# Kernel tuning notes

Measured on AMD Instinct MI355X. Metric: run time of the kernel, lower is better.

Reference implementation:

```python
import jax, jax.numpy as jnp
import numpy as np

B, D, H, V, T = 64, 1024, 1024, 32000, 20
SOS = 0  # word_to_idx['<SOS>']


def setup_inputs() -> dict:
    key = jax.random.key(0)
    ks = jax.random.split(key, 6)
    s = 0.02
    return {
        "latent_vector": jax.random.normal(ks[0], (B, D), jnp.float32),
        "W_proj": jax.random.normal(ks[1], (H, D), jnp.float32) * s,
        "b_proj": jnp.zeros((H,), jnp.float32),
        "emb": jax.random.normal(ks[2], (V, H), jnp.float32) * s,
        "W_ih": jax.random.normal(ks[3], (3 * H, H), jnp.float32) * s,
        "b_ih": jnp.zeros((3 * H,), jnp.float32),
        "W_hh": jax.random.normal(ks[4], (3 * H, H), jnp.float32) * s,
        "b_hh": jnp.zeros((3 * H,), jnp.float32),
        "W_out": jax.random.normal(ks[5], (V, H), jnp.float32) * s,
        "b_out": jnp.zeros((V,), jnp.float32),
    }


def _gru_cell(x, h, W_ih, b_ih, W_hh, b_hh):
    # PyTorch GRU cell gate math
    gi = x @ W_ih.T + b_ih  # [B, 3H]
    gh = h @ W_hh.T + b_hh  # [B, 3H]
    i_r, i_z, i_n = jnp.split(gi, 3, axis=-1)
    h_r, h_z, h_n = jnp.split(gh, 3, axis=-1)
    r = jax.nn.sigmoid(i_r + h_r)
    z = jax.nn.sigmoid(i_z + h_z)
    n = jnp.tanh(i_n + r * h_n)
    return (1.0 - z) * n + z * h


def reference(latent_vector, W_proj, b_proj, emb, W_ih, b_ih, W_hh, b_hh, W_out, b_out):
    batch = latent_vector.shape[0]
    h = latent_vector @ W_proj.T + b_proj  # init_hidden: [B, H]
    tok0 = jnp.full((batch,), SOS, dtype=jnp.int32)

    def step(carry, _):
        tok, h = carry
        x = emb[tok]                                  # embedding lookup [B, H]
        h = _gru_cell(x, h, W_ih, b_ih, W_hh, b_hh)   # GRU step
        logits = h @ W_out.T + b_out                  # [B, V]
        tok = jnp.argmax(logits, axis=-1).astype(jnp.int32)  # topk(1) greedy
        return (tok, h), tok

    (_, h_final), toks = jax.lax.scan(step, (tok0, h), None, length=T)
    # torch: stack(outputs, dim=1).squeeze() -> [B, T]; hidden -> [1, B, H]
    return toks.T, h_final[None, :, :]
```

## Files before the change

### kernel.cpp

```cpp
#include <hip/hip_runtime.h>
#include <stdint.h>

#define B_ 64
#define D_ 1024
#define H_ 1024
#define V_ 32000
#define T_ 20

typedef __attribute__((ext_vector_type(8))) __bf16 bf16x8;
typedef __attribute__((ext_vector_type(4))) float f32x4;

__device__ __forceinline__ uint32_t ord_of_float(float x) {
    uint32_t u = __float_as_uint(x);
    return (u & 0x80000000u) ? ~u : (u | 0x80000000u);
}

__device__ __forceinline__ unsigned long long shfl_xor_u64(unsigned long long x, int m) {
    return (unsigned long long)__shfl_xor((long long)x, m, 64);
}

__device__ __forceinline__ void split_bf16(float f, unsigned short* hi, unsigned short* lo) {
    uint32_t u = __float_as_uint(f);
    uint32_t rh = (u + 0x7FFFu + ((u >> 16) & 1u)) >> 16;
    *hi = (unsigned short)rh;
    float fl = f - __uint_as_float(rh << 16);
    uint32_t ul = __float_as_uint(fl);
    uint32_t rl = (ul + 0x7FFFu + ((ul >> 16) & 1u)) >> 16;
    *lo = (unsigned short)rl;
}

__global__ __launch_bounds__(256) void k_init_hidden(
    const float* __restrict__ latent, const float* __restrict__ Wp,
    const float* __restrict__ bp, float* __restrict__ h0)
{
    int gw = (blockIdx.x * 256 + threadIdx.x) >> 6;
    int lane = threadIdx.x & 63;
    int j = gw >> 6;
    int b = gw & 63;
    const float4* a4 = (const float4*)(latent + b * D_);
    const float4* w4 = (const float4*)(Wp + (size_t)j * D_);
    float s = 0.f;
#pragma unroll
    for (int i = 0; i < 4; i++) {
        float4 a = a4[lane + 64 * i];
        float4 w = w4[lane + 64 * i];
        s += a.x * w.x + a.y * w.y + a.z * w.z + a.w * w.w;
    }
#pragma unroll
    for (int off = 32; off; off >>= 1) s += __shfl_down(s, off, 64);
    if (lane == 0) h0[b * H_ + j] = s + bp[j];
}

#define LSTRIDE 72

__global__ __launch_bounds__(256) void k_gates_gemm(
    const float* __restrict__ emb, const int* __restrict__ tok, int use_sos,
    const float* __restrict__ hprev, const float* __restrict__ Wih,
    const float* __restrict__ Whh, float* __restrict__ gbuf)
{
    __shared__ unsigned short Ahi[64 * LSTRIDE], Alo[64 * LSTRIDE];
    __shared__ unsigned short Bhi[64 * LSTRIDE], Blo[64 * LSTRIDE];
    int tid = threadIdx.x;
    int lane = tid & 63;
    int wv = tid >> 6;
    int blk = blockIdx.x;
    int jt = blk % 48;
    int rest = blk / 48;
    int half = rest & 1;
    int ks = rest >> 1;
    int kbase = ks * 512;

    const float* W = half ? Whh : Wih;

    int srow = tid >> 2;
    int scol = (tid & 3) * 16;
    const float* arow;
    if (half == 0) {
        int xr = use_sos ? 0 : tok[srow];
        arow = emb + (size_t)xr * H_;
    } else {
        arow = hprev + srow * H_;
    }
    const float* asrc = arow + kbase + scol;
    const float* bsrc = W + (size_t)(jt * 64 + srow) * H_ + kbase + scol;

    unsigned short* ahd = Ahi + srow * LSTRIDE + scol;
    unsigned short* ald = Alo + srow * LSTRIDE + scol;
    unsigned short* bhd = Bhi + srow * LSTRIDE + scol;
    unsigned short* bld = Blo + srow * LSTRIDE + scol;

    f32x4 acc[4];
#pragma unroll
    for (int i = 0; i < 4; i++) acc[i] = (f32x4){0.f, 0.f, 0.f, 0.f};

    int arow_f = wv * 16 + (lane & 15);
    int koff = (lane >> 4) * 8;

    for (int kc = 0; kc < 512; kc += 64) {
        float4 av[4], bv[4];
#pragma unroll
        for (int i = 0; i < 4; i++) {
            av[i] = *(const float4*)(asrc + kc + 4 * i);
            bv[i] = *(const float4*)(bsrc + kc + 4 * i);
        }
        __syncthreads();
#pragma unroll
        for (int i = 0; i < 4; i++) {
            split_bf16(av[i].x, ahd + 4 * i + 0, ald + 4 * i + 0);
            split_bf16(av[i].y, ahd + 4 * i + 1, ald + 4 * i + 1);
            split_bf16(av[i].z, ahd + 4 * i + 2, ald + 4 * i + 2);
            split_bf16(av[i].w, ahd + 4 * i + 3, ald + 4 * i + 3);
            split_bf16(bv[i].x, bhd + 4 * i + 0, bld + 4 * i + 0);
            split_bf16(bv[i].y, bhd + 4 * i + 1, bld + 4 * i + 1);
            split_bf16(bv[i].z, bhd + 4 * i + 2, bld + 4 * i + 2);
            split_bf16(bv[i].w, bhd + 4 * i + 3, bld + 4 * i + 3);
        }
        __syncthreads();
        bf16x8 ah0 = *(const bf16x8*)(Ahi + arow_f * LSTRIDE + koff);
        bf16x8 ah1 = *(const bf16x8*)(Ahi + arow_f * LSTRIDE + 32 + koff);
        bf16x8 al0 = *(const bf16x8*)(Alo + arow_f * LSTRIDE + koff);
        bf16x8 al1 = *(const bf16x8*)(Alo + arow_f * LSTRIDE + 32 + koff);
#pragma unroll
        for (int tv = 0; tv < 4; tv++) {
            int brow = tv * 16 + (lane & 15);
            bf16x8 bh0 = *(const bf16x8*)(Bhi + brow * LSTRIDE + koff);
            bf16x8 bh1 = *(const bf16x8*)(Bhi + brow * LSTRIDE + 32 + koff);
            bf16x8 bl0 = *(const bf16x8*)(Blo + brow * LSTRIDE + koff);
            bf16x8 bl1 = *(const bf16x8*)(Blo + brow * LSTRIDE + 32 + koff);
            acc[tv] = __builtin_amdgcn_mfma_f32_16x16x32_bf16(ah0, bh0, acc[tv], 0, 0, 0);
            acc[tv] = __builtin_amdgcn_mfma_f32_16x16x32_bf16(ah1, bh1, acc[tv], 0, 0, 0);
            acc[tv] = __builtin_amdgcn_mfma_f32_16x16x32_bf16(al0, bh0, acc[tv], 0, 0, 0);
            acc[tv] = __builtin_amdgcn_mfma_f32_16x16x32_bf16(al1, bh1, acc[tv], 0, 0, 0);
            acc[tv] = __builtin_amdgcn_mfma_f32_16x16x32_bf16(ah0, bl0, acc[tv], 0, 0, 0);
            acc[tv] = __builtin_amdgcn_mfma_f32_16x16x32_bf16(ah1, bl1, acc[tv], 0, 0, 0);
        }
    }

    int col = lane & 15;
    int quad = lane >> 4;
    float* og = gbuf + (size_t)((ks * 2 + half) * 64) * 3072;
#pragma unroll
    for (int tv = 0; tv < 4; tv++) {
#pragma unroll
        for (int r = 0; r < 4; r++) {
            int b = wv * 16 + quad * 4 + r;
            og[(size_t)b * 3072 + jt * 64 + tv * 16 + col] = acc[tv][r];
        }
    }
}

__global__ __launch_bounds__(256) void k_gru_elem(
    const float* __restrict__ gbuf, const float* __restrict__ bih,
    const float* __restrict__ bhh, const float* __restrict__ hprev,
    float* __restrict__ hnext)
{
    int idx = blockIdx.x * 256 + threadIdx.x;
    int b = idx >> 10;
    int j = idx & 1023;
    const float* g00 = gbuf + (size_t)b * 3072;
    const float* g01 = gbuf + (size_t)(64 + b) * 3072;
    const float* g10 = gbuf + (size_t)(128 + b) * 3072;
    const float* g11 = gbuf + (size_t)(192 + b) * 3072;
    float ir = g00[j] + g10[j] + bih[j];
    float hr = g01[j] + g11[j] + bhh[j];
    float iz = g00[H_ + j] + g10[H_ + j] + bih[H_ + j];
    float hz = g01[H_ + j] + g11[H_ + j] + bhh[H_ + j];
    float in_ = g00[2 * H_ + j] + g10[2 * H_ + j] + bih[2 * H_ + j];
    float hn = g01[2 * H_ + j] + g11[2 * H_ + j] + bhh[2 * H_ + j];
    float r = 1.f / (1.f + expf(-(ir + hr)));
    float z = 1.f / (1.f + expf(-(iz + hz)));
    float n = tanhf(in_ + r * hn);
    float hp = hprev[idx];
    hnext[idx] = (1.f - z) * n + z * hp;
}

__global__ __launch_bounds__(256) void k_logits_argmax(
    const float* __restrict__ hcur, const float* __restrict__ Wout,
    const float* __restrict__ bout, unsigned long long* __restrict__ partials,
    int nblk)
{
    __shared__ unsigned short Ahi[64 * LSTRIDE], Alo[64 * LSTRIDE];
    __shared__ unsigned short Bhi[64 * LSTRIDE], Blo[64 * LSTRIDE];
    int tid = threadIdx.x;
    int lane = tid & 63;
    int wv = tid >> 6;
    int vbase = blockIdx.x * 64;

    int srow = tid >> 2;
    int scol = (tid & 3) * 16;
    const float* asrc = hcur + srow * H_ + scol;
    const float* bsrc = Wout + (size_t)(vbase + srow) * H_ + scol;
    unsigned short* ahd = Ahi + srow * LSTRIDE + scol;
    unsigned short* ald = Alo + srow * LSTRIDE + scol;
    unsigned short* bhd = Bhi + srow * LSTRIDE + scol;
    unsigned short* bld = Blo + srow * LSTRIDE + scol;

    f32x4 acc[4];
#pragma unroll
    for (int i = 0; i < 4; i++) acc[i] = (f32x4){0.f, 0.f, 0.f, 0.f};

    int arow = wv * 16 + (lane & 15);
    int koff = (lane >> 4) * 8;

    for (int kc = 0; kc < H_; kc += 64) {
        float4 av[4], bv[4];
#pragma unroll
        for (int i = 0; i < 4; i++) {
            av[i] = *(const float4*)(asrc + kc + 4 * i);
            bv[i] = *(const float4*)(bsrc + kc + 4 * i);
        }
        __syncthreads();
#pragma unroll
        for (int i = 0; i < 4; i++) {
            split_bf16(av[i].x, ahd + 4 * i + 0, ald + 4 * i + 0);
            split_bf16(av[i].y, ahd + 4 * i + 1, ald + 4 * i + 1);
            split_bf16(av[i].z, ahd + 4 * i + 2, ald + 4 * i + 2);
            split_bf16(av[i].w, ahd + 4 * i + 3, ald + 4 * i + 3);
            split_bf16(bv[i].x, bhd + 4 * i + 0, bld + 4 * i + 0);
            split_bf16(bv[i].y, bhd + 4 * i + 1, bld + 4 * i + 1);
            split_bf16(bv[i].z, bhd + 4 * i + 2, bld + 4 * i + 2);
            split_bf16(bv[i].w, bhd + 4 * i + 3, bld + 4 * i + 3);
        }
        __syncthreads();
        bf16x8 ah0 = *(const bf16x8*)(Ahi + arow * LSTRIDE + koff);
        bf16x8 ah1 = *(const bf16x8*)(Ahi + arow * LSTRIDE + 32 + koff);
        bf16x8 al0 = *(const bf16x8*)(Alo + arow * LSTRIDE + koff);
        bf16x8 al1 = *(const bf16x8*)(Alo + arow * LSTRIDE + 32 + koff);
#pragma unroll
        for (int tv = 0; tv < 4; tv++) {
            int brow = tv * 16 + (lane & 15);
            bf16x8 bh0 = *(const bf16x8*)(Bhi + brow * LSTRIDE + koff);
            bf16x8 bh1 = *(const bf16x8*)(Bhi + brow * LSTRIDE + 32 + koff);
            bf16x8 bl0 = *(const bf16x8*)(Blo + brow * LSTRIDE + koff);
            bf16x8 bl1 = *(const bf16x8*)(Blo + brow * LSTRIDE + 32 + koff);
            acc[tv] = __builtin_amdgcn_mfma_f32_16x16x32_bf16(ah0, bh0, acc[tv], 0, 0, 0);
            acc[tv] = __builtin_amdgcn_mfma_f32_16x16x32_bf16(ah1, bh1, acc[tv], 0, 0, 0);
            acc[tv] = __builtin_amdgcn_mfma_f32_16x16x32_bf16(al0, bh0, acc[tv], 0, 0, 0);
            acc[tv] = __builtin_amdgcn_mfma_f32_16x16x32_bf16(al1, bh1, acc[tv], 0, 0, 0);
            acc[tv] = __builtin_amdgcn_mfma_f32_16x16x32_bf16(ah0, bl0, acc[tv], 0, 0, 0);
            acc[tv] = __builtin_amdgcn_mfma_f32_16x16x32_bf16(ah1, bl1, acc[tv], 0, 0, 0);
        }
    }

    int col = lane & 15;
    int quad = lane >> 4;
    unsigned long long kmax[4] = {0ull, 0ull, 0ull, 0ull};
#pragma unroll
    for (int tv = 0; tv < 4; tv++) {
        int v = vbase + tv * 16 + col;
        float bo = bout[v];
#pragma unroll
        for (int r = 0; r < 4; r++) {
            float lg = acc[tv][r] + bo;
            unsigned long long key = ((unsigned long long)ord_of_float(lg) << 32)
                                   | (unsigned long long)(0x7FFFFFFFu - (uint32_t)v);
            if (key > kmax[r]) kmax[r] = key;
        }
    }
#pragma unroll
    for (int r = 0; r < 4; r++) {
        unsigned long long k = kmax[r];
#pragma unroll
        for (int off = 1; off < 16; off <<= 1) {
            unsigned long long o = shfl_xor_u64(k, off);
            if (o > k) k = o;
        }
        kmax[r] = k;
    }
    if (col == 0) {
#pragma unroll
        for (int r = 0; r < 4; r++) {
            int b = wv * 16 + quad * 4 + r;
            partials[(size_t)b * nblk + blockIdx.x] = kmax[r];
        }
    }
}

__global__ __launch_bounds__(64) void k_token(
    const unsigned long long* __restrict__ partials, int nblk,
    int* __restrict__ tok, float* __restrict__ out_tokens, int t)
{
    int b = blockIdx.x;
    int lane = threadIdx.x;
    unsigned long long k = 0ull;
    for (int i = lane; i < nblk; i += 64) {
        unsigned long long p = partials[(size_t)b * nblk + i];
        if (p > k) k = p;
    }
#pragma unroll
    for (int off = 32; off; off >>= 1) {
        unsigned long long o = shfl_xor_u64(k, off);
        if (o > k) k = o;
    }
    if (lane == 0) {
        int v = (int)(0x7FFFFFFFu - (uint32_t)(k & 0xFFFFFFFFull));
        tok[b] = v;
        out_tokens[b * T_ + t] = (float)v;
    }
}

__global__ __launch_bounds__(256) void k_copy_h(const float* __restrict__ h,
                                               float* __restrict__ out)
{
    int i = (blockIdx.x * 256 + threadIdx.x) * 4;
    *(float4*)(out + i) = *(const float4*)(h + i);
}

extern "C" void kernel_launch(void* const* d_in, const int* in_sizes, int n_in,
                              void* d_out, int out_size, void* d_ws, size_t ws_size,
                              hipStream_t stream)
{
    const float* latent = (const float*)d_in[0];
    const float* Wp     = (const float*)d_in[1];
    const float* bp     = (const float*)d_in[2];
    const float* emb    = (const float*)d_in[3];
    const float* Wih    = (const float*)d_in[4];
    const float* bih    = (const float*)d_in[5];
    const float* Whh    = (const float*)d_in[6];
    const float* bhh    = (const float*)d_in[7];
    const float* Wout   = (const float*)d_in[8];
    const float* bout   = (const float*)d_in[9];
    float* out = (float*)d_out;

    char* ws = (char*)d_ws;
    float* h0 = (float*)ws;
    float* h1 = (float*)(ws + 262144);
    int* tok  = (int*)(ws + 524288);
    unsigned long long* partials = (unsigned long long*)(ws + 525312);
    float* gbuf = (float*)(ws + 786432);
    const int NBLK = V_ / 64;

    k_init_hidden<<<16384, 256, 0, stream>>>(latent, Wp, bp, h0);

    float* hp = h0;
    float* hn = h1;
    for (int t = 0; t < T_; t++) {
        k_gates_gemm<<<192, 256, 0, stream>>>(emb, tok, t == 0 ? 1 : 0,
                                              hp, Wih, Whh, gbuf);
        k_gru_elem<<<256, 256, 0, stream>>>(gbuf, bih, bhh, hp, hn);
        k_logits_argmax<<<NBLK, 256, 0, stream>>>(hn, Wout, bout, partials, NBLK);
        k_token<<<B_, 64, 0, stream>>>(partials, NBLK, tok, out, t);
        float* tmp = hp; hp = hn; hn = tmp;
    }
    k_copy_h<<<64, 256, 0, stream>>>(hp, out + B_ * T_);
}
```

Measured before the change: 1.390 ms.

## Pre-split weights to bf16 hi/lo once and stream via async LDS double buffering

The fp32 weights W_ih, W_hh and W_out are split into bf16 hi/lo arrays once per call, and hidden states and embeddings are split when they are produced. Per-step GEMMs therefore read half-width bf16 data straight into swizzled, double-buffered LDS with global_load_lds, instead of reloading fp32 and re-splitting every tile on every timestep. The A operands are read directly from global memory. In exchange there is an extra up-front pass over about 140MB of weights and a much larger workspace.

```diff
diff --git a/kernel.cpp b/kernel.cpp
--- a/kernel.cpp
+++ b/kernel.cpp
@@ -6,6 +6,7 @@
 #define H_ 1024
 #define V_ 32000
 #define T_ 20
+#define SOS_ 0
 
 typedef __attribute__((ext_vector_type(8))) __bf16 bf16x8;
 typedef __attribute__((ext_vector_type(4))) float f32x4;
@@ -29,9 +30,31 @@
     *lo = (unsigned short)rl;
 }
 
+__device__ __forceinline__ void gload_lds16(const void* g, void* l) {
+    __builtin_amdgcn_global_load_lds(
+        (const __attribute__((address_space(1))) void*)g,
+        (__attribute__((address_space(3))) void*)l, 16, 0, 0);
+}
+
+__global__ __launch_bounds__(256) void k_split_w(const float* __restrict__ src,
+    unsigned short* __restrict__ hi, unsigned short* __restrict__ lo, int n4)
+{
+    int i = blockIdx.x * 256 + threadIdx.x;
+    if (i >= n4) return;
+    float4 v = ((const float4*)src)[i];
+    ushort4 h, l;
+    split_bf16(v.x, &h.x, &l.x);
+    split_bf16(v.y, &h.y, &l.y);
+    split_bf16(v.z, &h.z, &l.z);
+    split_bf16(v.w, &h.w, &l.w);
+    ((ushort4*)hi)[i] = h;
+    ((ushort4*)lo)[i] = l;
+}
+
 __global__ __launch_bounds__(256) void k_init_hidden(
     const float* __restrict__ latent, const float* __restrict__ Wp,
-    const float* __restrict__ bp, float* __restrict__ h0)
+    const float* __restrict__ bp, float* __restrict__ h0,
+    unsigned short* __restrict__ hhi, unsigned short* __restrict__ hlo)
 {
     int gw = (blockIdx.x * 256 + threadIdx.x) >> 6;
     int lane = threadIdx.x & 63;
@@ -48,18 +71,39 @@
     }
 #pragma unroll
     for (int off = 32; off; off >>= 1) s += __shfl_down(s, off, 64);
-    if (lane == 0) h0[b * H_ + j] = s + bp[j];
-}
-
-#define LSTRIDE 72
-
-__global__ __launch_bounds__(256) void k_gates_gemm(
-    const float* __restrict__ emb, const int* __restrict__ tok, int use_sos,
-    const float* __restrict__ hprev, const float* __restrict__ Wih,
-    const float* __restrict__ Whh, float* __restrict__ gbuf)
-{
-    __shared__ unsigned short Ahi[64 * LSTRIDE], Alo[64 * LSTRIDE];
-    __shared__ unsigned short Bhi[64 * LSTRIDE], Blo[64 * LSTRIDE];
+    if (lane == 0) {
+        float v = s + bp[j];
+        h0[b * H_ + j] = v;
+        unsigned short h_, l_;
+        split_bf16(v, &h_, &l_);
+        hhi[b * H_ + j] = h_;
+        hlo[b * H_ + j] = l_;
+    }
+}
+
+__global__ __launch_bounds__(256) void k_prep_x0(const float* __restrict__ emb,
+    unsigned short* __restrict__ xhi, unsigned short* __restrict__ xlo)
+{
+    int b = blockIdx.x;
+    int tid = threadIdx.x;
+    float4 v4 = *(const float4*)(emb + (size_t)SOS_ * H_ + tid * 4);
+    ushort4 h, l;
+    split_bf16(v4.x, &h.x, &l.x);
+    split_bf16(v4.y, &h.y, &l.y);
+    split_bf16(v4.z, &h.z, &l.z);
+    split_bf16(v4.w, &h.w, &l.w);
+    *(ushort4*)(xhi + (size_t)b * H_ + tid * 4) = h;
+    *(ushort4*)(xlo + (size_t)b * H_ + tid * 4) = l;
+}
+
+__global__ __launch_bounds__(256) void k_gates_gemm2(
+    const unsigned short* __restrict__ xhi, const unsigned short* __restrict__ xlo,
+    const unsigned short* __restrict__ hhi, const unsigned short* __restrict__ hlo,
+    const unsigned short* __restrict__ wihh, const unsigned short* __restrict__ wihl,
+    const unsigned short* __restrict__ whhh, const unsigned short* __restrict__ whhl,
+    float* __restrict__ gbuf)
+{
+    __shared__ __align__(128) char Bsm[2][16384];
     int tid = threadIdx.x;
     int lane = tid & 63;
     int wv = tid >> 6;
@@ -69,64 +113,60 @@
     int half = rest & 1;
     int ks = rest >> 1;
     int kbase = ks * 512;
-
-    const float* W = half ? Whh : Wih;
-
-    int srow = tid >> 2;
-    int scol = (tid & 3) * 16;
-    const float* arow;
-    if (half == 0) {
-        int xr = use_sos ? 0 : tok[srow];
-        arow = emb + (size_t)xr * H_;
-    } else {
-        arow = hprev + srow * H_;
-    }
-    const float* asrc = arow + kbase + scol;
-    const float* bsrc = W + (size_t)(jt * 64 + srow) * H_ + kbase + scol;
-
-    unsigned short* ahd = Ahi + srow * LSTRIDE + scol;
-    unsigned short* ald = Alo + srow * LSTRIDE + scol;
-    unsigned short* bhd = Bhi + srow * LSTRIDE + scol;
-    unsigned short* bld = Blo + srow * LSTRIDE + scol;
+    int row0 = jt * 64;
+
+    const unsigned short* Ahi_g = half ? hhi : xhi;
+    const unsigned short* Alo_g = half ? hlo : xlo;
+    const unsigned short* Bhi_g = half ? whhh : wihh;
+    const unsigned short* Blo_g = half ? whhl : wihl;
+
+    int r0 = wv * 8 + (lane >> 3);
+    int r1 = r0 + 32;
+    int kslt = (lane & 7) * 16;
+    size_t so0 = (size_t)(row0 + r0) * 2048 + (size_t)(kslt ^ ((r0 & 7) << 4));
+    size_t so1 = (size_t)(row0 + r1) * 2048 + (size_t)(kslt ^ ((r1 & 7) << 4));
+
+    int mrow = wv * 16 + (lane & 15);
+    int koff = (lane >> 4) * 8;
+    int kb = koff * 2;
 
     f32x4 acc[4];
 #pragma unroll
     for (int i = 0; i < 4; i++) acc[i] = (f32x4){0.f, 0.f, 0.f, 0.f};
 
-    int arow_f = wv * 16 + (lane & 15);
-    int koff = (lane >> 4) * 8;
-
-    for (int kc = 0; kc < 512; kc += 64) {
-        float4 av[4], bv[4];
-#pragma unroll
-        for (int i = 0; i < 4; i++) {
-            av[i] = *(const float4*)(asrc + kc + 4 * i);
-            bv[i] = *(const float4*)(bsrc + kc + 4 * i);
-        }
-        __syncthreads();
-#pragma unroll
-        for (int i = 0; i < 4; i++) {
-            split_bf16(av[i].x, ahd + 4 * i + 0, ald + 4 * i + 0);
-            split_bf16(av[i].y, ahd + 4 * i + 1, ald + 4 * i + 1);
-            split_bf16(av[i].z, ahd + 4 * i + 2, ald + 4 * i + 2);
-            split_bf16(av[i].w, ahd + 4 * i + 3, ald + 4 * i + 3);
-            split_bf16(bv[i].x, bhd + 4 * i + 0, bld + 4 * i + 0);
-            split_bf16(bv[i].y, bhd + 4 * i + 1, bld + 4 * i + 1);
-            split_bf16(bv[i].z, bhd + 4 * i + 2, bld + 4 * i + 2);
-            split_bf16(bv[i].w, bhd + 4 * i + 3, bld + 4 * i + 3);
-        }
-        __syncthreads();
-        bf16x8 ah0 = *(const bf16x8*)(Ahi + arow_f * LSTRIDE + koff);
-        bf16x8 ah1 = *(const bf16x8*)(Ahi + arow_f * LSTRIDE + 32 + koff);
-        bf16x8 al0 = *(const bf16x8*)(Alo + arow_f * LSTRIDE + koff);
-        bf16x8 al1 = *(const bf16x8*)(Alo + arow_f * LSTRIDE + 32 + koff);
+    auto stage = [&](int BUF, int KC) {
+        const char* bh = (const char*)Bhi_g + (size_t)KC * 2;
+        const char* bl = (const char*)Blo_g + (size_t)KC * 2;
+        char* base = Bsm[BUF] + wv * 1024;
+        gload_lds16(bh + so0, base);
+        gload_lds16(bh + so1, base + 4096);
+        gload_lds16(bl + so0, base + 8192);
+        gload_lds16(bl + so1, base + 12288);
+    };
+
+    int buf = 0;
+    stage(0, kbase);
+    __syncthreads();
+    for (int it = 0; it < 8; ++it) {
+        int kc = kbase + it * 64;
+        if (it < 7) stage(buf ^ 1, kc + 64);
+        const unsigned short* ap = Ahi_g + (size_t)mrow * 1024 + kc + koff;
+        const unsigned short* alp = Alo_g + (size_t)mrow * 1024 + kc + koff;
+        bf16x8 ah0 = *(const bf16x8*)ap;
+        bf16x8 ah1 = *(const bf16x8*)(ap + 32);
+        bf16x8 al0 = *(const bf16x8*)alp;
+        bf16x8 al1 = *(const bf16x8*)(alp + 32);
+        const char* bhp = Bsm[buf];
+        const char* blp = Bsm[buf] + 8192;
 #pragma unroll
         for (int tv = 0; tv < 4; tv++) {
             int brow = tv * 16 + (lane & 15);
-            bf16x8 bh0 = *(const bf16x8*)(Bhi + brow * LSTRIDE + koff);
-            bf16x8 bh1 = *(const bf16x8*)(Bhi + brow * LSTRIDE + 32 + koff);
-            bf16x8 bl0 = *(const bf16x8*)(Blo + brow * LSTRIDE + koff);
-            bf16x8 bl1 = *(const bf16x8*)(Blo + brow * LSTRIDE + 32 + koff);
+            int swz = (brow & 7) << 4;
+            int ro = brow * 128;
+            bf16x8 bh0 = *(const bf16x8*)(bhp + ro + (kb ^ swz));
+            bf16x8 bh1 = *(const bf16x8*)(bhp + ro + ((kb + 64) ^ swz));
+            bf16x8 bl0 = *(const bf16x8*)(blp + ro + (kb ^ swz));
+            bf16x8 bl1 = *(const bf16x8*)(blp + ro + ((kb + 64) ^ swz));
             acc[tv] = __builtin_amdgcn_mfma_f32_16x16x32_bf16(ah0, bh0, acc[tv], 0, 0, 0);
             acc[tv] = __builtin_amdgcn_mfma_f32_16x16x32_bf16(ah1, bh1, acc[tv], 0, 0, 0);
             acc[tv] = __builtin_amdgcn_mfma_f32_16x16x32_bf16(al0, bh0, acc[tv], 0, 0, 0);
@@ -134,6 +174,8 @@
             acc[tv] = __builtin_amdgcn_mfma_f32_16x16x32_bf16(ah0, bl0, acc[tv], 0, 0, 0);
             acc[tv] = __builtin_amdgcn_mfma_f32_16x16x32_bf16(ah1, bl1, acc[tv], 0, 0, 0);
         }
+        __syncthreads();
+        buf ^= 1;
     }
 
     int col = lane & 15;
@@ -149,10 +191,11 @@
     }
 }
 
-__global__ __launch_bounds__(256) void k_gru_elem(
+__global__ __launch_bounds__(256) void k_gru_elem2(
     const float* __restrict__ gbuf, const float* __restrict__ bih,
     const float* __restrict__ bhh, const float* __restrict__ hprev,
-    float* __restrict__ hnext)
+    float* __restrict__ hnext, unsigned short* __restrict__ hnhi,
+    unsigned short* __restrict__ hnlo)
 {
     int idx = blockIdx.x * 256 + threadIdx.x;
     int b = idx >> 10;
@@ -171,68 +214,73 @@
     float z = 1.f / (1.f + expf(-(iz + hz)));
     float n = tanhf(in_ + r * hn);
     float hp = hprev[idx];
-    hnext[idx] = (1.f - z) * n + z * hp;
-}
-
-__global__ __launch_bounds__(256) void k_logits_argmax(
-    const float* __restrict__ hcur, const float* __restrict__ Wout,
+    float v = (1.f - z) * n + z * hp;
+    hnext[idx] = v;
+    unsigned short h_, l_;
+    split_bf16(v, &h_, &l_);
+    hnhi[idx] = h_;
+    hnlo[idx] = l_;
+}
+
+__global__ __launch_bounds__(256) void k_logits_argmax2(
+    const unsigned short* __restrict__ hhi, const unsigned short* __restrict__ hlo,
+    const unsigned short* __restrict__ wouth, const unsigned short* __restrict__ woutl,
     const float* __restrict__ bout, unsigned long long* __restrict__ partials,
     int nblk)
 {
-    __shared__ unsigned short Ahi[64 * LSTRIDE], Alo[64 * LSTRIDE];
-    __shared__ unsigned short Bhi[64 * LSTRIDE], Blo[64 * LSTRIDE];
+    __shared__ __align__(128) char Bsm[2][16384];
     int tid = threadIdx.x;
     int lane = tid & 63;
     int wv = tid >> 6;
-    int vbase = blockIdx.x * 64;
-
-    int srow = tid >> 2;
-    int scol = (tid & 3) * 16;
-    const float* asrc = hcur + srow * H_ + scol;
-    const float* bsrc = Wout + (size_t)(vbase + srow) * H_ + scol;
-    unsigned short* ahd = Ahi + srow * LSTRIDE + scol;
-    unsigned short* ald = Alo + srow * LSTRIDE + scol;
-    unsigned short* bhd = Bhi + srow * LSTRIDE + scol;
-    unsigned short* bld = Blo + srow * LSTRIDE + scol;
+    int row0 = blockIdx.x * 64;
+
+    int r0 = wv * 8 + (lane >> 3);
+    int r1 = r0 + 32;
+    int kslt = (lane & 7) * 16;
+    size_t so0 = (size_t)(row0 + r0) * 2048 + (size_t)(kslt ^ ((r0 & 7) << 4));
+    size_t so1 = (size_t)(row0 + r1) * 2048 + (size_t)(kslt ^ ((r1 & 7) << 4));
+
+    int mrow = wv * 16 + (lane & 15);
+    int koff = (lane >> 4) * 8;
+    int kb = koff * 2;
 
     f32x4 acc[4];
 #pragma unroll
     for (int i = 0; i < 4; i++) acc[i] = (f32x4){0.f, 0.f, 0.f, 0.f};
 
-    int arow = wv * 16 + (lane & 15);
-    int koff = (lane >> 4) * 8;
-
-    for (int kc = 0; kc < H_; kc += 64) {
-        float4 av[4], bv[4];
-#pragma unroll
-        for (int i = 0; i < 4; i++) {
-            av[i] = *(const float4*)(asrc + kc + 4 * i);
-            bv[i] = *(const float4*)(bsrc + kc + 4 * i);
-        }
-        __syncthreads();
-#pragma unroll
-        for (int i = 0; i < 4; i++) {
-            split_bf16(av[i].x, ahd + 4 * i + 0, ald + 4 * i + 0);
-            split_bf16(av[i].y, ahd + 4 * i + 1, ald + 4 * i + 1);
-            split_bf16(av[i].z, ahd + 4 * i + 2, ald + 4 * i + 2);
-            split_bf16(av[i].w, ahd + 4 * i + 3, ald + 4 * i + 3);
-            split_bf16(bv[i].x, bhd + 4 * i + 0, bld + 4 * i + 0);
-            split_bf16(bv[i].y, bhd + 4 * i + 1, bld + 4 * i + 1);
-            split_bf16(bv[i].z, bhd + 4 * i + 2, bld + 4 * i + 2);
-            split_bf16(bv[i].w, bhd + 4 * i + 3, bld + 4 * i + 3);
-        }
-        __syncthreads();
-        bf16x8 ah0 = *(const bf16x8*)(Ahi + arow * LSTRIDE + koff);
-        bf16x8 ah1 = *(const bf16x8*)(Ahi + arow * LSTRIDE + 32 + koff);
-        bf16x8 al0 = *(const bf16x8*)(Alo + arow * LSTRIDE + koff);
-        bf16x8 al1 = *(const bf16x8*)(Alo + arow * LSTRIDE + 32 + koff);
+    auto stage = [&](int BUF, int KC) {
+        const char* bh = (const char*)wouth + (size_t)KC * 2;
+        const char* bl = (const char*)woutl + (size_t)KC * 2;
+        char* base = Bsm[BUF] + wv * 1024;
+        gload_lds16(bh + so0, base);
+        gload_lds16(bh + so1, base + 4096);
+        gload_lds16(bl + so0, base + 8192);
+        gload_lds16(bl + so1, base + 12288);
+    };
+
+    int buf = 0;
+    stage(0, 0);
+    __syncthreads();
+    for (int it = 0; it < 16; ++it) {
+        int kc = it * 64;
+        if (it < 15) stage(buf ^ 1, kc + 64);
+        const unsigned short* ap = hhi + (size_t)mrow * 1024 + kc + koff;
+        const unsigned short* alp = hlo + (size_t)mrow * 1024 + kc + koff;
+        bf16x8 ah0 = *(const bf16x8*)ap;
+        bf16x8 ah1 = *(const bf16x8*)(ap + 32);
+        bf16x8 al0 = *(const bf16x8*)alp;
+        bf16x8 al1 = *(const bf16x8*)(alp + 32);
+        const char* bhp = Bsm[buf];
+        const char* blp = Bsm[buf] + 8192;
 #pragma unroll
         for (int tv = 0; tv < 4; tv++) {
             int brow = tv * 16 + (lane & 15);
-            bf16x8 bh0 = *(const bf16x8*)(Bhi + brow * LSTRIDE + koff);
-            bf16x8 bh1 = *(const bf16x8*)(Bhi + brow * LSTRIDE + 32 + koff);
-            bf16x8 bl0 = *(const bf16x8*)(Blo + brow * LSTRIDE + koff);
-            bf16x8 bl1 = *(const bf16x8*)(Blo + brow * LSTRIDE + 32 + koff);
+            int swz = (brow & 7) << 4;
+            int ro = brow * 128;
+            bf16x8 bh0 = *(const bf16x8*)(bhp + ro + (kb ^ swz));
+            bf16x8 bh1 = *(const bf16x8*)(bhp + ro + ((kb + 64) ^ swz));
+            bf16x8 bl0 = *(const bf16x8*)(blp + ro + (kb ^ swz));
+            bf16x8 bl1 = *(const bf16x8*)(blp + ro + ((kb + 64) ^ swz));
             acc[tv] = __builtin_amdgcn_mfma_f32_16x16x32_bf16(ah0, bh0, acc[tv], 0, 0, 0);
             acc[tv] = __builtin_amdgcn_mfma_f32_16x16x32_bf16(ah1, bh1, acc[tv], 0, 0, 0);
             acc[tv] = __builtin_amdgcn_mfma_f32_16x16x32_bf16(al0, bh0, acc[tv], 0, 0, 0);
@@ -240,6 +288,8 @@
             acc[tv] = __builtin_amdgcn_mfma_f32_16x16x32_bf16(ah0, bl0, acc[tv], 0, 0, 0);
             acc[tv] = __builtin_amdgcn_mfma_f32_16x16x32_bf16(ah1, bl1, acc[tv], 0, 0, 0);
         }
+        __syncthreads();
+        buf ^= 1;
     }
 
     int col = lane & 15;
@@ -247,7 +297,7 @@
     unsigned long long kmax[4] = {0ull, 0ull, 0ull, 0ull};
 #pragma unroll
     for (int tv = 0; tv < 4; tv++) {
-        int v = vbase + tv * 16 + col;
+        int v = row0 + tv * 16 + col;
         float bo = bout[v];
 #pragma unroll
         for (int r = 0; r < 4; r++) {
@@ -276,27 +326,43 @@
     }
 }
 
-__global__ __launch_bounds__(64) void k_token(
+__global__ __launch_bounds__(256) void k_token2(
     const unsigned long long* __restrict__ partials, int nblk,
-    int* __restrict__ tok, float* __restrict__ out_tokens, int t)
-{
+    int* __restrict__ tok, float* __restrict__ out_tokens, int t,
+    const float* __restrict__ emb,
+    unsigned short* __restrict__ xhi, unsigned short* __restrict__ xlo)
+{
+    __shared__ int s_tok;
     int b = blockIdx.x;
-    int lane = threadIdx.x;
-    unsigned long long k = 0ull;
-    for (int i = lane; i < nblk; i += 64) {
-        unsigned long long p = partials[(size_t)b * nblk + i];
-        if (p > k) k = p;
-    }
-#pragma unroll
-    for (int off = 32; off; off >>= 1) {
-        unsigned long long o = shfl_xor_u64(k, off);
-        if (o > k) k = o;
-    }
-    if (lane == 0) {
-        int v = (int)(0x7FFFFFFFu - (uint32_t)(k & 0xFFFFFFFFull));
-        tok[b] = v;
-        out_tokens[b * T_ + t] = (float)v;
-    }
+    int tid = threadIdx.x;
+    if (tid < 64) {
+        unsigned long long k = 0ull;
+        for (int i = tid; i < nblk; i += 64) {
+            unsigned long long p = partials[(size_t)b * nblk + i];
+            if (p > k) k = p;
+        }
+#pragma unroll
+        for (int off = 32; off; off >>= 1) {
+            unsigned long long o = shfl_xor_u64(k, off);
+            if (o > k) k = o;
+        }
+        if (tid == 0) {
+            int v = (int)(0x7FFFFFFFu - (uint32_t)(k & 0xFFFFFFFFull));
+            tok[b] = v;
+            out_tokens[b * T_ + t] = (float)v;
+            s_tok = v;
+        }
+    }
+    __syncthreads();
+    int row = s_tok;
+    float4 v4 = *(const float4*)(emb + (size_t)row * H_ + tid * 4);
+    ushort4 h, l;
+    split_bf16(v4.x, &h.x, &l.x);
+    split_bf16(v4.y, &h.y, &l.y);
+    split_bf16(v4.z, &h.z, &l.z);
+    split_bf16(v4.w, &h.w, &l.w);
+    *(ushort4*)(xhi + (size_t)b * H_ + tid * 4) = h;
+    *(ushort4*)(xlo + (size_t)b * H_ + tid * 4) = l;
 }
 
 __global__ __launch_bounds__(256) void k_copy_h(const float* __restrict__ h,
@@ -323,24 +389,45 @@
     float* out = (float*)d_out;
 
     char* ws = (char*)d_ws;
-    float* h0 = (float*)ws;
-    float* h1 = (float*)(ws + 262144);
-    int* tok  = (int*)(ws + 524288);
+    float* h0   = (float*)(ws + 0);
+    float* h1   = (float*)(ws + 262144);
+    int* tok    = (int*)(ws + 524288);
     unsigned long long* partials = (unsigned long long*)(ws + 525312);
-    float* gbuf = (float*)(ws + 786432);
+    float* gbuf = (float*)(ws + 787456);
+    unsigned short* hhi0 = (unsigned short*)(ws + 3933184);
+    unsigned short* hlo0 = (unsigned short*)(ws + 4064256);
+    unsigned short* hhi1 = (unsigned short*)(ws + 4195328);
+    unsigned short* hlo1 = (unsigned short*)(ws + 4326400);
+    unsigned short* xhi  = (unsigned short*)(ws + 4457472);
+    unsigned short* xlo  = (unsigned short*)(ws + 4588544);
+    unsigned short* wihh = (unsigned short*)(ws + 4719616);
+    unsigned short* wihl = (unsigned short*)(ws + 11011072);
+    unsigned short* whhh = (unsigned short*)(ws + 17302528);
+    unsigned short* whhl = (unsigned short*)(ws + 23593984);
+    unsigned short* wouth = (unsigned short*)(ws + 29885440);
+    unsigned short* woutl = (unsigned short*)(ws + 95421440);
+
     const int NBLK = V_ / 64;
 
-    k_init_hidden<<<16384, 256, 0, stream>>>(latent, Wp, bp, h0);
-
-    float* hp = h0;
-    float* hn = h1;
+    k_split_w<<<3072, 256, 0, stream>>>(Wih, wihh, wihl, 3 * H_ * H_ / 4);
+    k_split_w<<<3072, 256, 0, stream>>>(Whh, whhh, whhl, 3 * H_ * H_ / 4);
+    k_split_w<<<32000, 256, 0, stream>>>(Wout, wouth, woutl, V_ * H_ / 4);
+
+    k_init_hidden<<<16384, 256, 0, stream>>>(latent, Wp, bp, h0, hhi0, hlo0);
+    k_prep_x0<<<64, 256, 0, stream>>>(emb, xhi, xlo);
+
+    float* hp = h0;  unsigned short* hphi = hhi0;  unsigned short* hplo = hlo0;
+    float* hn = h1;  unsigned short* hnhi = hhi1;  unsigned short* hnlo = hlo1;
     for (int t = 0; t < T_; t++) {
-        k_gates_gemm<<<192, 256, 0, stream>>>(emb, tok, t == 0 ? 1 : 0,
-                                              hp, Wih, Whh, gbuf);
-        k_gru_elem<<<256, 256, 0, stream>>>(gbuf, bih, bhh, hp, hn);
-        k_logits_argmax<<<NBLK, 256, 0, stream>>>(hn, Wout, bout, partials, NBLK);
-        k_token<<<B_, 64, 0, stream>>>(partials, NBLK, tok, out, t);
-        float* tmp = hp; hp = hn; hn = tmp;
+        k_gates_gemm2<<<192, 256, 0, stream>>>(xhi, xlo, hphi, hplo,
+                                               wihh, wihl, whhh, whhl, gbuf);
+        k_gru_elem2<<<256, 256, 0, stream>>>(gbuf, bih, bhh, hp, hn, hnhi, hnlo);
+        k_logits_argmax2<<<NBLK, 256, 0, stream>>>(hnhi, hnlo, wouth, woutl,
+                                                   bout, partials, NBLK);
+        k_token2<<<B_, 256, 0, stream>>>(partials, NBLK, tok, out, t, emb, xhi, xlo);
+        { float* tf = hp; hp = hn; hn = tf; }
+        { unsigned short* ts = hphi; hphi = hnhi; hnhi = ts; }
+        { unsigned short* ts = hplo; hplo = hnlo; hnlo = ts; }
     }
     k_copy_h<<<64, 256, 0, stream>>>(hp, out + B_ * T_);
 }
```

Measured after the change: 1.265 ms. -9.0%, faster.
